# Kernel optimization log

Measured on AMD Instinct MI355X. Metric: run time of the kernel, lower is better.

## Reference

```python
import jax, jax.numpy as jnp
import numpy as np

# Renderer constants matching neural_renderer.Renderer(camera_mode='look',
# light_intensity_ambient=0.5, light_intensity_directional=0.5,
# light_direction=[0,0,1], viewing_angle=45) with image_size=256.
IMG = 256
TEX = 6
VIEW_ANGLE_DEG = 45.0
EYE = np.array([0.0, 0.0, -2.0], dtype=np.float32)          # camera position (look mode)
CAM_DIR = np.array([0.0, 0.0, 1.0], dtype=np.float32)       # camera_direction
CAM_UP = np.array([0.0, 1.0, 0.0], dtype=np.float32)        # camera_up
LIGHT_DIR = np.array([0.0, 0.0, 1.0], dtype=np.float32)
AMBIENT = 0.5
DIRECTIONAL = 0.5
EPS = 1e-8


def setup_inputs() -> dict:
    key = jax.random.key(0)
    k1, k2, k3 = jax.random.split(key, 3)
    # mesh roughly centered at origin; camera sits at z=-2 looking toward +z
    vertices = 0.5 * jax.random.normal(k1, (1, 400, 3), dtype=jnp.float32)
    faces = jax.random.randint(k2, (1, 640, 3), 0, 400, dtype=jnp.int64)
    textures = 0.5 * jax.random.normal(k3, (1, 640, TEX, TEX, TEX, 3), dtype=jnp.float32)
    return {"vertices": vertices, "faces": faces, "textures": textures}


def _normalize(v):
    return v / (jnp.linalg.norm(v, axis=-1, keepdims=True) + EPS)


def reference(vertices, faces, textures):
    v = vertices[0]                 # [N,3]
    f = faces[0]                    # [F,3] int
    tex = jnp.tanh(textures[0])     # [F,T,T,T,3]  (torch.tanh(textures))

    fv = v[f]                       # [F,3,3] per-face vertex positions (world)

    # ---- lighting (ambient + directional, white lights) ----
    n = jnp.cross(fv[:, 1] - fv[:, 0], fv[:, 2] - fv[:, 0])  # [F,3]
    n = _normalize(n)
    diff = jax.nn.relu(n @ jnp.asarray(LIGHT_DIR))           # [F]
    light = AMBIENT + DIRECTIONAL * diff                     # [F] (same for rgb)

    # ---- 'look' camera transform ----
    z_ax = _normalize(jnp.asarray(CAM_DIR))
    x_ax = _normalize(jnp.cross(jnp.asarray(CAM_UP), z_ax))
    y_ax = jnp.cross(z_ax, x_ax)
    R = jnp.stack([x_ax, y_ax, z_ax], axis=0)                # [3,3]
    vc = (fv - jnp.asarray(EYE)) @ R.T                       # [F,3,3] camera space

    # ---- perspective projection ----
    wfov = jnp.tan(jnp.deg2rad(VIEW_ANGLE_DEG)).astype(jnp.float32)
    zc = vc[..., 2]                                          # [F,3] depth
    xy = vc[..., :2] / (zc[..., None] * wfov + EPS)          # [F,3,2] in [-1,1]

    # ---- rasterize: barycentric coords per pixel per face ----
    ps = (jnp.arange(IMG, dtype=jnp.float32) + 0.5) / IMG * 2.0 - 1.0
    px, py = jnp.meshgrid(ps, -ps, indexing="xy")            # image y flipped
    pts = jnp.stack([px.ravel(), py.ravel()], axis=-1)       # [P,2]

    v0 = xy[:, 0]                                            # [F,2]
    d = xy[:, 1] - v0                                        # [F,2]
    e = xy[:, 2] - v0                                        # [F,2]
    det = d[:, 0] * e[:, 1] - d[:, 1] * e[:, 0]              # [F]
    det_ok = jnp.abs(det) > 1e-8
    det_s = jnp.where(det_ok, det, 1.0)

    q = pts[:, None, :] - v0[None, :, :]                     # [P,F,2]
    w1 = (q[..., 0] * e[:, 1] - q[..., 1] * e[:, 0]) / det_s # [P,F]
    w2 = (d[:, 0] * q[..., 1] - d[:, 1] * q[..., 0]) / det_s # [P,F]
    w0 = 1.0 - w1 - w2

    inside = (w0 >= 0) & (w1 >= 0) & (w2 >= 0) & det_ok[None, :]
    depth = w0 * zc[:, 0] + w1 * zc[:, 1] + w2 * zc[:, 2]    # [P,F]
    visible = inside & (depth > 0)

    # ---- z-buffer: nearest visible face per pixel ----
    big = jnp.float32(1e30)
    dmask = jnp.where(visible, depth, big)                   # [P,F]
    idx = jnp.argmin(dmask, axis=1)                          # [P]
    valid = jnp.take_along_axis(visible, idx[:, None], axis=1)[:, 0]  # [P]

    gather = lambda a: jnp.take_along_axis(a, idx[:, None], axis=1)[:, 0]
    b0, b1, b2 = gather(w0), gather(w1), gather(w2)          # [P] each

    # ---- texture lookup: nearest cell in TxTxT cube by barycentric coords ----
    ti = lambda b: jnp.clip((b * TEX).astype(jnp.int32), 0, TEX - 1)
    i0, i1, i2 = ti(b0), ti(b1), ti(b2)
    col = tex[idx, i0, i1, i2]                               # [P,3]
    col = col * light[idx][:, None]                          # shade

    img = jnp.where(valid[:, None], col, 0.0)                # [P,3]
    img = img.reshape(IMG, IMG, 3).transpose(2, 0, 1)[None]  # [1,3,H,W]
    return img
```

## Files before the change

### kernel.cpp

```cpp
#include <hip/hip_runtime.h>
#include <math.h>

#define NF   640
#define IMGN 256
#define NPIX (IMGN * IMGN)
#define TEXN 6
#define NV   400
#define TPB  512
#define PXW  64
#define NCH  8
#define CHF  (NF / NCH)

__global__ __launch_bounds__(TPB) void render_kernel(
    const float* __restrict__ verts,
    const int*   __restrict__ faces,
    const float* __restrict__ tex,
    float* __restrict__ out)
{
#pragma clang fp contract(off)
    __shared__ float  sPX[NV], sPY[NV], sZ[NV];
    __shared__ float4 fA[NF];
    __shared__ float4 fB[NF];
    __shared__ float2 fZ[NF];
    __shared__ unsigned short sListW[NCH][CHF];
    __shared__ unsigned short sMerged[NF];
    __shared__ int   sCnt[NCH];
    __shared__ float rD[NCH][PXW];
    __shared__ int   rI[NCH][PXW];

    const float EPSf = 1e-8f;
    const int tid  = (int)threadIdx.x;
    const int wid  = tid >> 6;
    const int lane = tid & 63;
    const int p0   = (int)blockIdx.x * PXW;
    const int pi   = p0 >> 8;
    const int pj0  = p0 & (IMGN - 1);

    const float by    = -(((pi + 0.5f) / (float)IMGN) * 2.0f - 1.0f);
    const float bxmin = ((pj0 + 0.5f) / (float)IMGN) * 2.0f - 1.0f;
    const float bxmax = ((pj0 + (PXW - 1) + 0.5f) / (float)IMGN) * 2.0f - 1.0f;

    if (tid < NV) {
        float x = verts[3 * tid], y = verts[3 * tid + 1], z = verts[3 * tid + 2];
        float z0 = z + 2.0f;
        float den = z0 * 1.0f + EPSf;
        sPX[tid] = x / den;
        sPY[tid] = y / den;
        sZ[tid]  = z0;
    }
    __syncthreads();

    const int fbeg = wid * CHF;
    int cnt = 0;
    for (int r = 0; r < 2; ++r) {
        int idx = r * 64 + lane;
        int f = fbeg + idx;
        bool pred = false;
        if (idx < CHF) {
            int ia = faces[3 * f + 0];
            int ib = faces[3 * f + 1];
            int ic = faces[3 * f + 2];
            float px0 = sPX[ia], py0 = sPY[ia], z0 = sZ[ia];
            float px1 = sPX[ib], py1 = sPY[ib], z1 = sZ[ib];
            float px2 = sPX[ic], py2 = sPY[ic], z2 = sZ[ic];

            float dx = px1 - px0, dy = py1 - py0;
            float ex = px2 - px0, ey = py2 - py0;
            float det = dx * ey - dy * ex;
            bool ok = fabsf(det) > 1e-8f;

            fA[f] = make_float4(px0, py0, ex, ey);
            fB[f] = make_float4(dx, dy, ok ? det : 1.0f, z0);
            fZ[f] = make_float2(z1, z2);

            if (ok) {
                float xmin = fminf(px0, fminf(px1, px2));
                float xmax = fmaxf(px0, fmaxf(px1, px2));
                float ymin = fminf(py0, fminf(py1, py2));
                float ymax = fmaxf(py0, fmaxf(py1, py2));
                float padx = (fmaxf(fabsf(xmin), fabsf(xmax)) + 1.0f) * 1e-6f;
                float pady = (fmaxf(fabsf(ymin), fabsf(ymax)) + 1.0f) * 1e-6f;
                pred = (ymin - pady <= by)    && (ymax + pady >= by) &&
                       (xmin - padx <= bxmax) && (xmax + padx >= bxmin);
            }
        }
        unsigned long long m = __ballot(pred);
        if (pred)
            sListW[wid][cnt + (int)__popcll(m & ((1ull << lane) - 1ull))] =
                (unsigned short)f;
        cnt += (int)__popcll(m);
    }
    if (lane == 0) sCnt[wid] = cnt;
    __syncthreads();

    int base = 0, total = 0;
    #pragma unroll
    for (int c = 0; c < NCH; ++c) {
        int cc = sCnt[c];
        if (c < wid) base += cc;
        total += cc;
    }
    for (int i = lane; i < cnt; i += 64)
        sMerged[base + i] = sListW[wid][i];
    __syncthreads();

    const float ppx = ((pj0 + lane + 0.5f) / (float)IMGN) * 2.0f - 1.0f;
    const float ppy = by;

    const int per = (total + NCH - 1) >> 3;
    const int kb  = wid * per;
    const int ke  = (kb + per < total) ? (kb + per) : total;

    float best = 1e30f;
    int   bi = -1;

    for (int k = kb; k < ke; ++k) {
        int f = (int)sMerged[k];
        float4 a = fA[f];
        float4 b = fB[f];
        float qx = ppx - a.x;
        float qy = ppy - a.y;
        float n1 = qx * a.w - qy * a.z;
        float n2 = b.x * qy - b.y * qx;
        bool pass = (b.z > 0.0f) ? (n1 >= 0.0f && n2 >= 0.0f)
                                 : (n1 <= 0.0f && n2 <= 0.0f);
        if (pass) {
            float w1 = n1 / b.z;
            float w2 = n2 / b.z;
            float w0 = (1.0f - w1) - w2;
            if (w0 >= 0.0f) {
                float2 zz = fZ[f];
                float depth = ((w0 * b.w) + (w1 * zz.x)) + (w2 * zz.y);
                if (depth > 0.0f && depth < best) {
                    best = depth; bi = f;
                }
            }
        }
    }

    rD[wid][lane] = best;
    rI[wid][lane] = bi;
    __syncthreads();

    if (tid < PXW) {
        float bd = rD[0][tid];
        int   fi = rI[0][tid];
        for (int c = 1; c < NCH; ++c) {
            float d = rD[c][tid];
            if (d < bd) { bd = d; fi = rI[c][tid]; }
        }

        int pp = p0 + tid;
        float r = 0.0f, g = 0.0f, b = 0.0f;
        if (fi >= 0) {
            float4 a2 = fA[fi];
            float4 b2 = fB[fi];
            float sx = ((pj0 + tid + 0.5f) / (float)IMGN) * 2.0f - 1.0f;
            float qx = sx - a2.x;
            float qy = by - a2.y;
            float n1 = qx * a2.w - qy * a2.z;
            float n2 = b2.x * qy - b2.y * qx;
            float w1 = n1 / b2.z;
            float w2 = n2 / b2.z;
            float w0 = (1.0f - w1) - w2;

            int ia = faces[3 * fi + 0];
            int ib = faces[3 * fi + 1];
            int ic = faces[3 * fi + 2];
            float ax = verts[3 * ia], ay = verts[3 * ia + 1], az = verts[3 * ia + 2];
            float bx = verts[3 * ib], byv = verts[3 * ib + 1], bz = verts[3 * ib + 2];
            float cx = verts[3 * ic], cy = verts[3 * ic + 1], cz = verts[3 * ic + 2];
            float e1x = bx - ax, e1y = byv - ay, e1z = bz - az;
            float e2x = cx - ax, e2y = cy - ay, e2z = cz - az;
            float nx = e1y * e2z - e1z * e2y;
            float ny = e1z * e2x - e1x * e2z;
            float nz = e1x * e2y - e1y * e2x;
            float nn = sqrtf((nx * nx + ny * ny) + nz * nz) + EPSf;
            float diff = nz / nn;
            diff = diff > 0.0f ? diff : 0.0f;
            float light = 0.5f + 0.5f * diff;

            int i0 = (int)(w0 * (float)TEXN);
            int i1 = (int)(w1 * (float)TEXN);
            int i2 = (int)(w2 * (float)TEXN);
            i0 = i0 < 0 ? 0 : (i0 > TEXN - 1 ? TEXN - 1 : i0);
            i1 = i1 < 0 ? 0 : (i1 > TEXN - 1 ? TEXN - 1 : i1);
            i2 = i2 < 0 ? 0 : (i2 > TEXN - 1 ? TEXN - 1 : i2);
            const float* tp = tex + (size_t)((((fi * TEXN + i0) * TEXN + i1) * TEXN + i2) * 3);
            r = tanhf(tp[0]) * light;
            g = tanhf(tp[1]) * light;
            b = tanhf(tp[2]) * light;
        }
        out[pp]            = r;
        out[NPIX + pp]     = g;
        out[2 * NPIX + pp] = b;
    }
}

extern "C" void kernel_launch(void* const* d_in, const int* in_sizes, int n_in,
                              void* d_out, int out_size, void* d_ws, size_t ws_size,
                              hipStream_t stream) {
    (void)in_sizes; (void)n_in; (void)d_ws; (void)ws_size; (void)out_size;
    const float* verts = (const float*)d_in[0];
    const int*   faces = (const int*)d_in[1];
    const float* tex   = (const float*)d_in[2];
    float*       out   = (float*)d_out;
    render_kernel<<<NPIX / PXW, TPB, 0, stream>>>(verts, faces, tex, out);
}
```

Before: 25.49 us.

## Widen blocks to 128 pixels with 16 warps, two pixels per lane

Each block now covers 128 pixels of a row using 1024 threads in 16 wavefronts. Each lane tests two pixels against every face it loads, so the face loads and the row-dependent terms are shared between both pixels. Face setup takes one pass per wavefront because each chunk now holds 40 faces. This halves the number of blocks that repeat per-block vertex projection and face binning, at the cost of coarser per-row culling, more register pressure, and a longer 16-way final reduction.

```diff
diff --git a/kernel.cpp b/kernel.cpp
--- a/kernel.cpp
+++ b/kernel.cpp
@@ -6,9 +6,9 @@
 #define NPIX (IMGN * IMGN)
 #define TEXN 6
 #define NV   400
-#define TPB  512
-#define PXW  64
-#define NCH  8
+#define TPB  1024
+#define PXW  128
+#define NCH  16
 #define CHF  (NF / NCH)
 
 __global__ __launch_bounds__(TPB) void render_kernel(
@@ -52,8 +52,8 @@
 
     const int fbeg = wid * CHF;
     int cnt = 0;
-    for (int r = 0; r < 2; ++r) {
-        int idx = r * 64 + lane;
+    {
+        int idx = lane;
         int f = fbeg + idx;
         bool pred = false;
         if (idx < CHF) {
@@ -86,9 +86,9 @@
         }
         unsigned long long m = __ballot(pred);
         if (pred)
-            sListW[wid][cnt + (int)__popcll(m & ((1ull << lane) - 1ull))] =
+            sListW[wid][(int)__popcll(m & ((1ull << lane) - 1ull))] =
                 (unsigned short)f;
-        cnt += (int)__popcll(m);
+        cnt = (int)__popcll(m);
     }
     if (lane == 0) sCnt[wid] = cnt;
     __syncthreads();
@@ -104,47 +104,70 @@
         sMerged[base + i] = sListW[wid][i];
     __syncthreads();
 
-    const float ppx = ((pj0 + lane + 0.5f) / (float)IMGN) * 2.0f - 1.0f;
-    const float ppy = by;
-
-    const int per = (total + NCH - 1) >> 3;
+    const float ppx0 = ((pj0 + lane      + 0.5f) / (float)IMGN) * 2.0f - 1.0f;
+    const float ppx1 = ((pj0 + lane + 64 + 0.5f) / (float)IMGN) * 2.0f - 1.0f;
+
+    const int per = (total + NCH - 1) >> 4;
     const int kb  = wid * per;
     const int ke  = (kb + per < total) ? (kb + per) : total;
 
-    float best = 1e30f;
-    int   bi = -1;
+    float best0 = 1e30f, best1 = 1e30f;
+    int   bi0 = -1,      bi1 = -1;
 
     for (int k = kb; k < ke; ++k) {
         int f = (int)sMerged[k];
         float4 a = fA[f];
         float4 b = fB[f];
-        float qx = ppx - a.x;
-        float qy = ppy - a.y;
-        float n1 = qx * a.w - qy * a.z;
-        float n2 = b.x * qy - b.y * qx;
-        bool pass = (b.z > 0.0f) ? (n1 >= 0.0f && n2 >= 0.0f)
-                                 : (n1 <= 0.0f && n2 <= 0.0f);
-        if (pass) {
-            float w1 = n1 / b.z;
-            float w2 = n2 / b.z;
-            float w0 = (1.0f - w1) - w2;
-            if (w0 >= 0.0f) {
-                float2 zz = fZ[f];
-                float depth = ((w0 * b.w) + (w1 * zz.x)) + (w2 * zz.y);
-                if (depth > 0.0f && depth < best) {
-                    best = depth; bi = f;
+        float2 zz = fZ[f];
+        float qy = by - a.y;
+        float t1 = qy * a.z;
+        float t2 = b.x * qy;
+        bool detpos = (b.z > 0.0f);
+
+        {
+            float qx = ppx0 - a.x;
+            float n1 = qx * a.w - t1;
+            float n2 = t2 - b.y * qx;
+            bool pass = detpos ? (n1 >= 0.0f && n2 >= 0.0f)
+                               : (n1 <= 0.0f && n2 <= 0.0f);
+            if (pass) {
+                float w1 = n1 / b.z;
+                float w2 = n2 / b.z;
+                float w0 = (1.0f - w1) - w2;
+                if (w0 >= 0.0f) {
+                    float depth = ((w0 * b.w) + (w1 * zz.x)) + (w2 * zz.y);
+                    if (depth > 0.0f && depth < best0) { best0 = depth; bi0 = f; }
                 }
             }
         }
-    }
-
-    rD[wid][lane] = best;
-    rI[wid][lane] = bi;
+        {
+            float qx = ppx1 - a.x;
+            float n1 = qx * a.w - t1;
+            float n2 = t2 - b.y * qx;
+            bool pass = detpos ? (n1 >= 0.0f && n2 >= 0.0f)
+                               : (n1 <= 0.0f && n2 <= 0.0f);
+            if (pass) {
+                float w1 = n1 / b.z;
+                float w2 = n2 / b.z;
+                float w0 = (1.0f - w1) - w2;
+                if (w0 >= 0.0f) {
+                    float depth = ((w0 * b.w) + (w1 * zz.x)) + (w2 * zz.y);
+                    if (depth > 0.0f && depth < best1) { best1 = depth; bi1 = f; }
+                }
+            }
+        }
+    }
+
+    rD[wid][lane]      = best0;
+    rI[wid][lane]      = bi0;
+    rD[wid][lane + 64] = best1;
+    rI[wid][lane + 64] = bi1;
     __syncthreads();
 
     if (tid < PXW) {
         float bd = rD[0][tid];
         int   fi = rI[0][tid];
+        #pragma unroll
         for (int c = 1; c < NCH; ++c) {
             float d = rD[c][tid];
             if (d < bd) { bd = d; fi = rI[c][tid]; }
```

Result: faster. 24.17 us (-5.2%).
